# Kernel tuning notes

Measured on AMD Instinct MI355X. Metric: run time of the kernel, lower is better.

## Reference

```python
import jax, jax.numpy as jnp
import numpy as np

TOPK = 20
BN_EPS = 1e-5
NEG_SLOPE = 0.2  # DGL GAT default leaky_relu slope


def setup_inputs() -> dict:
    B, N, Ft, D = 128, 512, 64, 64
    key = jax.random.key(0)
    ks = jax.random.split(key, 6)
    return {
        "data": jax.random.normal(ks[0], (B, N, Ft), jnp.float32),
        "emb": jax.random.normal(ks[1], (N, D), jnp.float32) * 0.5,
        "fc_w": jax.random.normal(ks[2], (D, Ft), jnp.float32) * (1.0 / np.sqrt(Ft)),
        "fc_b": jnp.zeros((D,), jnp.float32),
        "attn_w": jax.random.normal(ks[3], (4 * D,), jnp.float32) * (1.0 / np.sqrt(4 * D)),
        "attn_b": jnp.zeros((), jnp.float32),
        "bn_gamma": jnp.ones((D,), jnp.float32),
        "bn_beta": jnp.zeros((D,), jnp.float32),
        "out_w": jax.random.normal(ks[4], (D,), jnp.float32) * (1.0 / np.sqrt(D)),
        "out_b": jnp.zeros((), jnp.float32),
    }


def reference(data, emb, fc_w, fc_b, attn_w, attn_b, bn_gamma, bn_beta, out_w, out_b):
    B, N, Ft = data.shape
    D = emb.shape[-1]

    # --- dynamic graph build from detached embeddings (cosine-sim topk) ---
    w = jax.lax.stop_gradient(emb)
    nrm = jnp.linalg.norm(w, axis=-1)
    cos = (w @ w.T) / (nrm[:, None] * nrm[None, :])      # [N, N]
    _, topk_idx = jax.lax.top_k(cos, TOPK)               # [N, TOPK]
    src = topk_idx.reshape(-1)                           # gated_j (message sources)
    dst = jnp.tile(jnp.arange(N), TOPK)                  # gated_i = arange(N).repeat(1,topk).flatten()

    # --- GAT layer: z = W x + b ; edge score from concat([z, emb]) at both ends ---
    z = jnp.einsum("bnf,df->bnd", data, fc_w) + fc_b     # [B, N, D]
    key_feat = jnp.concatenate([z, jnp.broadcast_to(emb, (B, N, D))], axis=-1)  # [B, N, 2D]
    a_src, a_dst = attn_w[: 2 * D], attn_w[2 * D :]
    s_src = jnp.einsum("bnd,d->bn", key_feat, a_src)
    s_dst = jnp.einsum("bnd,d->bn", key_feat, a_dst)
    e = jax.nn.leaky_relu(s_src[:, src] + s_dst[:, dst] + attn_b, NEG_SLOPE)    # [B, E]

    # segment softmax over incoming edges of each dst node (same edges every batch)
    m = jnp.full((B, N), -jnp.inf, e.dtype).at[:, dst].max(e)
    p = jnp.exp(e - m[:, dst])
    denom = jnp.zeros((B, N), e.dtype).at[:, dst].add(p)
    alpha = p / denom[:, dst]                            # [B, E]

    # scatter-aggregate messages
    h = jnp.zeros_like(z).at[:, dst].add(alpha[..., None] * z[:, src])          # [B, N, D]

    # --- trailing dense: mul by embedding, BatchNorm1d over channel D, relu, linear ---
    rst = h * emb[None]                                  # [B, N, D]
    mu = rst.mean(axis=(0, 1))
    var = rst.var(axis=(0, 1))
    rst = jax.nn.relu((rst - mu) / jnp.sqrt(var + BN_EPS) * bn_gamma + bn_beta)
    out = jnp.einsum("bnd,d->bn", rst, out_w) + out_b    # [B, N]
    return out
```

## Files before the change

kernel.cpp:

```cpp
#include <hip/hip_runtime.h>
#include <hip/hip_bf16.h>

#define NN 512
#define DD 64
#define TOPK 20
#define BB 128

__global__ __launch_bounds__(64) void k1_topk(const float* __restrict__ emb,
                                              const float* __restrict__ attn_w,
                                              int* __restrict__ topk,
                                              float* __restrict__ es_src,
                                              float* __restrict__ es_dst) {
    const int i = blockIdx.x;
    const int lane = threadIdx.x;
    const float4* e4 = (const float4*)emb;

    double dot[8] = {0,0,0,0,0,0,0,0};
    double dj [8] = {0,0,0,0,0,0,0,0};
    double di = 0.0;

    for (int c = 0; c < 16; ++c) {
        float4 wi4 = e4[i * 16 + c];
        double wx = wi4.x, wy = wi4.y, wz = wi4.z, ww = wi4.w;
        di += wx * wx; di += wy * wy; di += wz * wz; di += ww * ww;
        #pragma unroll
        for (int r = 0; r < 8; ++r) {
            float4 v = e4[(lane * 8 + r) * 16 + c];
            double vx = v.x, vy = v.y, vz = v.z, vw = v.w;
            dot[r] += wx * vx; dot[r] += wy * vy; dot[r] += wz * vz; dot[r] += ww * vw;
            dj [r] += vx * vx; dj [r] += vy * vy; dj [r] += vz * vz; dj [r] += vw * vw;
        }
    }
    const double nrm_i = sqrt(di);
    double v[8];
    #pragma unroll
    for (int r = 0; r < 8; ++r) v[r] = dot[r] / (nrm_i * sqrt(dj[r]));

    for (int k = 0; k < TOPK; ++k) {
        double bv = v[0]; int br = 0;
        #pragma unroll
        for (int r = 1; r < 8; ++r) if (v[r] > bv) { bv = v[r]; br = r; }
        int bi = lane * 8 + br;
        #pragma unroll
        for (int off = 32; off > 0; off >>= 1) {
            double ov = __shfl_xor(bv, off);
            int    oi = __shfl_xor(bi, off);
            if (ov > bv || (ov == bv && oi < bi)) { bv = ov; bi = oi; }
        }
        if (lane == 0) topk[i * TOPK + k] = bi;
        if ((bi >> 3) == lane) v[bi & 7] = -1e300;
    }

    float wf = emb[i * 64 + lane];
    float v1 = wf * attn_w[64 + lane];
    float v2 = wf * attn_w[192 + lane];
    #pragma unroll
    for (int off = 32; off > 0; off >>= 1) {
        v1 += __shfl_xor(v1, off);
        v2 += __shfl_xor(v2, off);
    }
    if (lane == 0) { es_src[i] = v1; es_dst[i] = v2; }
}

__global__ __launch_bounds__(256) void k2_gemm(const float* __restrict__ data,
                                               const float* __restrict__ fc_w,
                                               const float* __restrict__ fc_b,
                                               const float* __restrict__ attn_w,
                                               const float* __restrict__ es_src,
                                               const float* __restrict__ es_dst,
                                               float* __restrict__ z,
                                               float* __restrict__ s_src,
                                               float* __restrict__ s_dst) {
    __shared__ float As[64][65];
    __shared__ float Ws[64][65];
    __shared__ float redA[64][17];
    __shared__ float redB[64][17];
    const int t = threadIdx.x;
    const long r0 = (long)blockIdx.x * 64;

    for (int idx = t; idx < 4096; idx += 256) {
        As[idx >> 6][idx & 63] = data[r0 * 64 + idx];
        Ws[idx >> 6][idx & 63] = fc_w[idx];
    }
    __syncthreads();

    const int tr = t >> 4, tc = t & 15;
    float acc[4][4] = {};
    for (int k = 0; k < 64; ++k) {
        float a[4], b[4];
        #pragma unroll
        for (int i = 0; i < 4; ++i) a[i] = As[tr * 4 + i][k];
        #pragma unroll
        for (int j = 0; j < 4; ++j) b[j] = Ws[tc * 4 + j][k];
        #pragma unroll
        for (int i = 0; i < 4; ++i)
            #pragma unroll
            for (int j = 0; j < 4; ++j) acc[i][j] += a[i] * b[j];
    }
    float bias[4], aw0[4], aw2[4];
    #pragma unroll
    for (int j = 0; j < 4; ++j) {
        bias[j] = fc_b[tc * 4 + j];
        aw0[j]  = attn_w[tc * 4 + j];
        aw2[j]  = attn_w[128 + tc * 4 + j];
    }
    #pragma unroll
    for (int i = 0; i < 4; ++i) {
        float zb[4];
        #pragma unroll
        for (int j = 0; j < 4; ++j) zb[j] = acc[i][j] + bias[j];
        float4 vv; vv.x = zb[0]; vv.y = zb[1]; vv.z = zb[2]; vv.w = zb[3];
        *(float4*)&z[(r0 + tr * 4 + i) * 64 + tc * 4] = vv;
        float pA = zb[0] * aw0[0] + zb[1] * aw0[1] + zb[2] * aw0[2] + zb[3] * aw0[3];
        float pB = zb[0] * aw2[0] + zb[1] * aw2[1] + zb[2] * aw2[2] + zb[3] * aw2[3];
        redA[tr * 4 + i][tc] = pA;
        redB[tr * 4 + i][tc] = pB;
    }
    __syncthreads();
    if (t < 64) {
        float sA = 0.f, sB = 0.f;
        #pragma unroll
        for (int k = 0; k < 16; ++k) { sA += redA[t][k]; sB += redB[t][k]; }
        const int n = (int)((r0 + t) & (NN - 1));
        s_src[r0 + t] = sA + es_src[n];
        s_dst[r0 + t] = sB + es_dst[n];
    }
}

__global__ __launch_bounds__(256) void k3_attn(const float* __restrict__ z,
                                               const float* __restrict__ s_src,
                                               const float* __restrict__ s_dst,
                                               const int* __restrict__ topk,
                                               const float* __restrict__ emb,
                                               const float* __restrict__ attn_b_p,
                                               float* __restrict__ rst,
                                               double* __restrict__ bsum,
                                               double* __restrict__ bsum2) {
    __shared__ float  zs[512 * 16];
    __shared__ double alf_pool[2560];
    __shared__ unsigned short sIdx[256 * 20];
    float* alf = (float*)alf_pool;

    const int b   = blockIdx.x >> 2;
    const int dq  = blockIdx.x & 3;
    const int doff = dq * 16;
    const int t   = threadIdx.x;
    const float attn_b = *attn_b_p;
    const long b512 = (long)b * NN;

    float4* zs4 = (float4*)zs;
    for (int m = t; m < 2048; m += 256) {
        const int n = m >> 2, c4 = m & 3;
        zs4[m] = *(const float4*)(z + (b512 + n) * 64 + doff + c4 * 4);
    }
    __syncthreads();

    const int g = t >> 4, c = t & 15;
    double sum1 = 0.0, sum2 = 0.0;

    for (int chunk = 0; chunk < 2; ++chunk) {
        {
            const int n = chunk * 256 + t;
            const float sd = s_dst[b512 + n];
            float ev[TOPK];
            float m0 = -1e30f;
            #pragma unroll
            for (int tt = 0; tt < TOPK; ++tt) {
                const int s = topk[n + tt * NN];
                sIdx[t * TOPK + tt] = (unsigned short)s;
                float e = s_src[b512 + s] + sd + attn_b;
                e = (e >= 0.f) ? e : 0.2f * e;
                ev[tt] = e;
                m0 = fmaxf(m0, e);
            }
            float dsum = 0.f;
            #pragma unroll
            for (int tt = 0; tt < TOPK; ++tt) { ev[tt] = __expf(ev[tt] - m0); dsum += ev[tt]; }
            const float inv = 1.0f / dsum;
            #pragma unroll
            for (int tt = 0; tt < TOPK; ++tt) alf[t * TOPK + tt] = ev[tt] * inv;
        }
        __syncthreads();

        for (int it = 0; it < 16; ++it) {
            const int nl = g * 16 + it;
            const int n  = chunk * 256 + nl;
            float acc = 0.f;
            #pragma unroll
            for (int tt = 0; tt < TOPK; ++tt) {
                acc += alf[nl * TOPK + tt] * zs[(int)sIdx[nl * TOPK + tt] * 16 + c];
            }
            const float r = acc * emb[n * 64 + doff + c];
            rst[(b512 + n) * 64 + doff + c] = r;
            sum1 += (double)r;
            sum2 += (double)r * (double)r;
        }
        __syncthreads();
    }

    double* r1 = alf_pool;
    double* r2 = alf_pool + 256;
    r1[t] = sum1; r2[t] = sum2;
    __syncthreads();
    if (t < 16) {
        double a = 0.0, bb = 0.0;
        for (int g2 = 0; g2 < 16; ++g2) { a += r1[g2 * 16 + t]; bb += r2[g2 * 16 + t]; }
        bsum [blockIdx.x * 16 + t] = a;
        bsum2[blockIdx.x * 16 + t] = bb;
    }
}

__global__ __launch_bounds__(64) void k4_bn(const double* __restrict__ bsum,
                                            const double* __restrict__ bsum2,
                                            const float* __restrict__ gamma,
                                            const float* __restrict__ beta,
                                            float* __restrict__ scaleArr,
                                            float* __restrict__ biasArr) {
    const int d = threadIdx.x;
    const int dq = d >> 4, c = d & 15;
    double s = 0.0, s2 = 0.0;
    for (int b = 0; b < BB; ++b) {
        const int blk = b * 4 + dq;
        s  += bsum [blk * 16 + c];
        s2 += bsum2[blk * 16 + c];
    }
    const double M = (double)BB * (double)NN;
    const double mu  = s / M;
    const double var = s2 / M - mu * mu;
    const float scale = (float)((double)gamma[d] / sqrt(var + 1e-5));
    scaleArr[d] = scale;
    biasArr[d]  = beta[d] - (float)mu * scale;
}

__global__ __launch_bounds__(256) void k5_out(const float* __restrict__ rst,
                                              const float* __restrict__ scaleArr,
                                              const float* __restrict__ biasArr,
                                              const float* __restrict__ out_w,
                                              const float* __restrict__ out_b_p,
                                              float* __restrict__ out) {
    const int wid = threadIdx.x >> 6, lane = threadIdx.x & 63;
    const long row = (long)blockIdx.x * 4 + wid;
    const float r = rst[row * 64 + lane];
    float v = fmaxf(r * scaleArr[lane] + biasArr[lane], 0.f) * out_w[lane];
    #pragma unroll
    for (int off = 32; off > 0; off >>= 1) v += __shfl_down(v, off);
    if (lane == 0) out[row] = v + *out_b_p;
}

extern "C" void kernel_launch(void* const* d_in, const int* in_sizes, int n_in,
                              void* d_out, int out_size, void* d_ws, size_t ws_size,
                              hipStream_t stream) {
    const float* data   = (const float*)d_in[0];
    const float* emb    = (const float*)d_in[1];
    const float* fc_w   = (const float*)d_in[2];
    const float* fc_b   = (const float*)d_in[3];
    const float* attn_w = (const float*)d_in[4];
    const float* attn_b = (const float*)d_in[5];
    const float* gamma  = (const float*)d_in[6];
    const float* beta   = (const float*)d_in[7];
    const float* out_w  = (const float*)d_in[8];
    const float* out_b  = (const float*)d_in[9];
    float* out = (float*)d_out;

    char* ws = (char*)d_ws;
    const long ROWS = (long)BB * NN;
    float*  z      = (float*) (ws + 0);
    float*  rst    = (float*) (ws + 16777216);
    float*  s_src  = (float*) (ws + 33554432);
    float*  s_dst  = (float*) (ws + 33816576);
    int*    topk   = (int*)   (ws + 34078720);
    float*  es_src = (float*) (ws + 34119680);
    float*  es_dst = (float*) (ws + 34121728);
    double* bsum   = (double*)(ws + 34123776);
    double* bsum2  = (double*)(ws + 34189312);
    float*  scaleA = (float*) (ws + 34254848);
    float*  biasA  = (float*) (ws + 34255104);

    k1_topk<<<NN, 64, 0, stream>>>(emb, attn_w, topk, es_src, es_dst);
    k2_gemm<<<(int)(ROWS / 64), 256, 0, stream>>>(data, fc_w, fc_b, attn_w, es_src, es_dst,
                                                  z, s_src, s_dst);
    k3_attn<<<BB * 4, 256, 0, stream>>>(z, s_src, s_dst, topk, emb, attn_b, rst, bsum, bsum2);
    k4_bn<<<1, 64, 0, stream>>>(bsum, bsum2, gamma, beta, scaleA, biasA);
    k5_out<<<(int)(ROWS / 4), 256, 0, stream>>>(rst, scaleA, biasA, out_w, out_b, out);
}
```

Before: 165.8 us.

## Fuse topk and GEMM kernels, vectorize attention aggregation and tail kernels

Merges the cosine top-k kernel and the projection GEMM into one launch, with extra blocks handling top-k four rows per block. Because the GEMM no longer depends on the top-k output, the embedding score terms move into the attention kernel. The GEMM now uses float4 LDS reads from a transposed weight tile. The attention aggregation switches to float4 per thread with reworked BN partial reductions, the BN reduce kernel is parallelized over 512 threads, and the output kernel handles four rows per wave. These changes aim to cut launch count, serialization and memory-instruction overhead, at the cost of more complex indexing and larger shared-memory reduction buffers.

```diff
diff --git a/kernel.cpp b/kernel.cpp
--- a/kernel.cpp
+++ b/kernel.cpp
@@ -6,130 +6,141 @@
 #define TOPK 20
 #define BB 128
 
-__global__ __launch_bounds__(64) void k1_topk(const float* __restrict__ emb,
-                                              const float* __restrict__ attn_w,
-                                              int* __restrict__ topk,
-                                              float* __restrict__ es_src,
-                                              float* __restrict__ es_dst) {
-    const int i = blockIdx.x;
-    const int lane = threadIdx.x;
-    const float4* e4 = (const float4*)emb;
-
-    double dot[8] = {0,0,0,0,0,0,0,0};
-    double dj [8] = {0,0,0,0,0,0,0,0};
-    double di = 0.0;
-
-    for (int c = 0; c < 16; ++c) {
-        float4 wi4 = e4[i * 16 + c];
-        double wx = wi4.x, wy = wi4.y, wz = wi4.z, ww = wi4.w;
-        di += wx * wx; di += wy * wy; di += wz * wz; di += ww * ww;
-        #pragma unroll
-        for (int r = 0; r < 8; ++r) {
-            float4 v = e4[(lane * 8 + r) * 16 + c];
-            double vx = v.x, vy = v.y, vz = v.z, vw = v.w;
-            dot[r] += wx * vx; dot[r] += wy * vy; dot[r] += wz * vz; dot[r] += ww * vw;
-            dj [r] += vx * vx; dj [r] += vy * vy; dj [r] += vz * vz; dj [r] += vw * vw;
-        }
-    }
-    const double nrm_i = sqrt(di);
-    double v[8];
-    #pragma unroll
-    for (int r = 0; r < 8; ++r) v[r] = dot[r] / (nrm_i * sqrt(dj[r]));
-
-    for (int k = 0; k < TOPK; ++k) {
-        double bv = v[0]; int br = 0;
-        #pragma unroll
-        for (int r = 1; r < 8; ++r) if (v[r] > bv) { bv = v[r]; br = r; }
-        int bi = lane * 8 + br;
-        #pragma unroll
-        for (int off = 32; off > 0; off >>= 1) {
-            double ov = __shfl_xor(bv, off);
-            int    oi = __shfl_xor(bi, off);
-            if (ov > bv || (ov == bv && oi < bi)) { bv = ov; bi = oi; }
-        }
-        if (lane == 0) topk[i * TOPK + k] = bi;
-        if ((bi >> 3) == lane) v[bi & 7] = -1e300;
-    }
-
-    float wf = emb[i * 64 + lane];
-    float v1 = wf * attn_w[64 + lane];
-    float v2 = wf * attn_w[192 + lane];
-    #pragma unroll
-    for (int off = 32; off > 0; off >>= 1) {
-        v1 += __shfl_xor(v1, off);
-        v2 += __shfl_xor(v2, off);
-    }
-    if (lane == 0) { es_src[i] = v1; es_dst[i] = v2; }
-}
-
-__global__ __launch_bounds__(256) void k2_gemm(const float* __restrict__ data,
-                                               const float* __restrict__ fc_w,
-                                               const float* __restrict__ fc_b,
-                                               const float* __restrict__ attn_w,
-                                               const float* __restrict__ es_src,
-                                               const float* __restrict__ es_dst,
-                                               float* __restrict__ z,
-                                               float* __restrict__ s_src,
-                                               float* __restrict__ s_dst) {
-    __shared__ float As[64][65];
-    __shared__ float Ws[64][65];
+__global__ __launch_bounds__(256) void k12_fused(const float* __restrict__ data,
+                                                 const float* __restrict__ fc_w,
+                                                 const float* __restrict__ fc_b,
+                                                 const float* __restrict__ emb,
+                                                 const float* __restrict__ attn_w,
+                                                 float* __restrict__ z,
+                                                 float* __restrict__ zsrc,
+                                                 float* __restrict__ zdst,
+                                                 int* __restrict__ topk,
+                                                 float* __restrict__ es_src,
+                                                 float* __restrict__ es_dst) {
+    __shared__ float As [64][68];
+    __shared__ float WsT[64][68];
     __shared__ float redA[64][17];
     __shared__ float redB[64][17];
     const int t = threadIdx.x;
-    const long r0 = (long)blockIdx.x * 64;
-
-    for (int idx = t; idx < 4096; idx += 256) {
-        As[idx >> 6][idx & 63] = data[r0 * 64 + idx];
-        Ws[idx >> 6][idx & 63] = fc_w[idx];
-    }
-    __syncthreads();
-
-    const int tr = t >> 4, tc = t & 15;
-    float acc[4][4] = {};
-    for (int k = 0; k < 64; ++k) {
-        float a[4], b[4];
-        #pragma unroll
-        for (int i = 0; i < 4; ++i) a[i] = As[tr * 4 + i][k];
-        #pragma unroll
-        for (int j = 0; j < 4; ++j) b[j] = Ws[tc * 4 + j][k];
-        #pragma unroll
-        for (int i = 0; i < 4; ++i)
-            #pragma unroll
-            for (int j = 0; j < 4; ++j) acc[i][j] += a[i] * b[j];
-    }
-    float bias[4], aw0[4], aw2[4];
-    #pragma unroll
-    for (int j = 0; j < 4; ++j) {
-        bias[j] = fc_b[tc * 4 + j];
-        aw0[j]  = attn_w[tc * 4 + j];
-        aw2[j]  = attn_w[128 + tc * 4 + j];
-    }
-    #pragma unroll
-    for (int i = 0; i < 4; ++i) {
-        float zb[4];
-        #pragma unroll
-        for (int j = 0; j < 4; ++j) zb[j] = acc[i][j] + bias[j];
-        float4 vv; vv.x = zb[0]; vv.y = zb[1]; vv.z = zb[2]; vv.w = zb[3];
-        *(float4*)&z[(r0 + tr * 4 + i) * 64 + tc * 4] = vv;
-        float pA = zb[0] * aw0[0] + zb[1] * aw0[1] + zb[2] * aw0[2] + zb[3] * aw0[3];
-        float pB = zb[0] * aw2[0] + zb[1] * aw2[1] + zb[2] * aw2[2] + zb[3] * aw2[3];
-        redA[tr * 4 + i][tc] = pA;
-        redB[tr * 4 + i][tc] = pB;
-    }
-    __syncthreads();
-    if (t < 64) {
-        float sA = 0.f, sB = 0.f;
-        #pragma unroll
-        for (int k = 0; k < 16; ++k) { sA += redA[t][k]; sB += redB[t][k]; }
-        const int n = (int)((r0 + t) & (NN - 1));
-        s_src[r0 + t] = sA + es_src[n];
-        s_dst[r0 + t] = sB + es_dst[n];
+
+    if (blockIdx.x < 1024) {
+        const long r0 = (long)blockIdx.x * 64;
+        const float4* data4 = (const float4*)data;
+        const float4* fcw4  = (const float4*)fc_w;
+
+        for (int m = t; m < 1024; m += 256) {
+            const int r = m >> 4, c4 = m & 15;
+            *(float4*)&As[r][c4 * 4] = data4[(r0 + r) * 16 + c4];
+        }
+        for (int m = t; m < 1024; m += 256) {
+            const int d = m >> 4, f4 = m & 15;
+            float4 v = fcw4[d * 16 + f4];
+            WsT[f4 * 4 + 0][d] = v.x;
+            WsT[f4 * 4 + 1][d] = v.y;
+            WsT[f4 * 4 + 2][d] = v.z;
+            WsT[f4 * 4 + 3][d] = v.w;
+        }
+        __syncthreads();
+
+        const int tr = t >> 4, tc = t & 15;
+        float acc[4][4] = {};
+        for (int k0 = 0; k0 < 64; k0 += 4) {
+            float4 a4[4], b4[4];
+            #pragma unroll
+            for (int i = 0; i < 4; ++i) a4[i] = *(float4*)&As[tr * 4 + i][k0];
+            #pragma unroll
+            for (int kk = 0; kk < 4; ++kk) b4[kk] = *(float4*)&WsT[k0 + kk][tc * 4];
+            #pragma unroll
+            for (int i = 0; i < 4; ++i) {
+                acc[i][0] += a4[i].x * b4[0].x + a4[i].y * b4[1].x + a4[i].z * b4[2].x + a4[i].w * b4[3].x;
+                acc[i][1] += a4[i].x * b4[0].y + a4[i].y * b4[1].y + a4[i].z * b4[2].y + a4[i].w * b4[3].y;
+                acc[i][2] += a4[i].x * b4[0].z + a4[i].y * b4[1].z + a4[i].z * b4[2].z + a4[i].w * b4[3].z;
+                acc[i][3] += a4[i].x * b4[0].w + a4[i].y * b4[1].w + a4[i].z * b4[2].w + a4[i].w * b4[3].w;
+            }
+        }
+        float bias[4], aw0[4], aw2[4];
+        #pragma unroll
+        for (int j = 0; j < 4; ++j) {
+            bias[j] = fc_b[tc * 4 + j];
+            aw0[j]  = attn_w[tc * 4 + j];
+            aw2[j]  = attn_w[128 + tc * 4 + j];
+        }
+        #pragma unroll
+        for (int i = 0; i < 4; ++i) {
+            float zb[4];
+            #pragma unroll
+            for (int j = 0; j < 4; ++j) zb[j] = acc[i][j] + bias[j];
+            float4 vv; vv.x = zb[0]; vv.y = zb[1]; vv.z = zb[2]; vv.w = zb[3];
+            *(float4*)&z[(r0 + tr * 4 + i) * 64 + tc * 4] = vv;
+            redA[tr * 4 + i][tc] = zb[0] * aw0[0] + zb[1] * aw0[1] + zb[2] * aw0[2] + zb[3] * aw0[3];
+            redB[tr * 4 + i][tc] = zb[0] * aw2[0] + zb[1] * aw2[1] + zb[2] * aw2[2] + zb[3] * aw2[3];
+        }
+        __syncthreads();
+        if (t < 64) {
+            float sA = 0.f, sB = 0.f;
+            #pragma unroll
+            for (int k = 0; k < 16; ++k) { sA += redA[t][k]; sB += redB[t][k]; }
+            zsrc[r0 + t] = sA;
+            zdst[r0 + t] = sB;
+        }
+    } else {
+        const int i = (blockIdx.x - 1024) * 4 + (t >> 6);
+        const int lane = t & 63;
+        const float4* e4 = (const float4*)emb;
+
+        double dot[8] = {0,0,0,0,0,0,0,0};
+        double dj [8] = {0,0,0,0,0,0,0,0};
+        double di = 0.0;
+
+        for (int c = 0; c < 16; ++c) {
+            float4 wi4 = e4[i * 16 + c];
+            double wx = wi4.x, wy = wi4.y, wz = wi4.z, ww = wi4.w;
+            di += wx * wx; di += wy * wy; di += wz * wz; di += ww * ww;
+            #pragma unroll
+            for (int r = 0; r < 8; ++r) {
+                float4 v = e4[(lane * 8 + r) * 16 + c];
+                double vx = v.x, vy = v.y, vz = v.z, vw = v.w;
+                dot[r] += wx * vx; dot[r] += wy * vy; dot[r] += wz * vz; dot[r] += ww * vw;
+                dj [r] += vx * vx; dj [r] += vy * vy; dj [r] += vz * vz; dj [r] += vw * vw;
+            }
+        }
+        const double nrm_i = sqrt(di);
+        double v[8];
+        #pragma unroll
+        for (int r = 0; r < 8; ++r) v[r] = dot[r] / (nrm_i * sqrt(dj[r]));
+
+        for (int k = 0; k < TOPK; ++k) {
+            double bv = v[0]; int br = 0;
+            #pragma unroll
+            for (int r = 1; r < 8; ++r) if (v[r] > bv) { bv = v[r]; br = r; }
+            int bi = lane * 8 + br;
+            #pragma unroll
+            for (int off = 32; off > 0; off >>= 1) {
+                double ov = __shfl_xor(bv, off);
+                int    oi = __shfl_xor(bi, off);
+                if (ov > bv || (ov == bv && oi < bi)) { bv = ov; bi = oi; }
+            }
+            if (lane == 0) topk[i * TOPK + k] = bi;
+            if ((bi >> 3) == lane) v[bi & 7] = -1e300;
+        }
+
+        float wf = emb[i * 64 + lane];
+        float v1 = wf * attn_w[64 + lane];
+        float v2 = wf * attn_w[192 + lane];
+        #pragma unroll
+        for (int off = 32; off > 0; off >>= 1) {
+            v1 += __shfl_xor(v1, off);
+            v2 += __shfl_xor(v2, off);
+        }
+        if (lane == 0) { es_src[i] = v1; es_dst[i] = v2; }
     }
 }
 
 __global__ __launch_bounds__(256) void k3_attn(const float* __restrict__ z,
-                                               const float* __restrict__ s_src,
-                                               const float* __restrict__ s_dst,
+                                               const float* __restrict__ zsrc,
+                                               const float* __restrict__ zdst,
+                                               const float* __restrict__ es_src,
+                                               const float* __restrict__ es_dst,
                                                const int* __restrict__ topk,
                                                const float* __restrict__ emb,
                                                const float* __restrict__ attn_b_p,
@@ -141,10 +152,10 @@
     __shared__ unsigned short sIdx[256 * 20];
     float* alf = (float*)alf_pool;
 
-    const int b   = blockIdx.x >> 2;
-    const int dq  = blockIdx.x & 3;
+    const int b    = blockIdx.x >> 2;
+    const int dq   = blockIdx.x & 3;
     const int doff = dq * 16;
-    const int t   = threadIdx.x;
+    const int t    = threadIdx.x;
     const float attn_b = *attn_b_p;
     const long b512 = (long)b * NN;
 
@@ -155,20 +166,21 @@
     }
     __syncthreads();
 
-    const int g = t >> 4, c = t & 15;
-    double sum1 = 0.0, sum2 = 0.0;
+    const int c4 = t & 3;
+    const int rq = t >> 2;
+    double s1[4] = {0,0,0,0}, s2[4] = {0,0,0,0};
 
     for (int chunk = 0; chunk < 2; ++chunk) {
         {
             const int n = chunk * 256 + t;
-            const float sd = s_dst[b512 + n];
+            const float sd = zdst[b512 + n] + es_dst[n] + attn_b;
             float ev[TOPK];
             float m0 = -1e30f;
             #pragma unroll
             for (int tt = 0; tt < TOPK; ++tt) {
                 const int s = topk[n + tt * NN];
                 sIdx[t * TOPK + tt] = (unsigned short)s;
-                float e = s_src[b512 + s] + sd + attn_b;
+                float e = zsrc[b512 + s] + es_src[s] + sd;
                 e = (e >= 0.f) ? e : 0.2f * e;
                 ev[tt] = e;
                 m0 = fmaxf(m0, e);
@@ -182,54 +194,74 @@
         }
         __syncthreads();
 
-        for (int it = 0; it < 16; ++it) {
-            const int nl = g * 16 + it;
+        #pragma unroll
+        for (int it = 0; it < 4; ++it) {
+            const int nl = it * 64 + rq;
             const int n  = chunk * 256 + nl;
-            float acc = 0.f;
+            float4 acc = {0.f, 0.f, 0.f, 0.f};
             #pragma unroll
             for (int tt = 0; tt < TOPK; ++tt) {
-                acc += alf[nl * TOPK + tt] * zs[(int)sIdx[nl * TOPK + tt] * 16 + c];
-            }
-            const float r = acc * emb[n * 64 + doff + c];
-            rst[(b512 + n) * 64 + doff + c] = r;
-            sum1 += (double)r;
-            sum2 += (double)r * (double)r;
+                const float a = alf[nl * TOPK + tt];
+                const float4 zv = zs4[(int)sIdx[nl * TOPK + tt] * 4 + c4];
+                acc.x += a * zv.x; acc.y += a * zv.y; acc.z += a * zv.z; acc.w += a * zv.w;
+            }
+            const float4 ev = *(const float4*)&emb[n * 64 + doff + c4 * 4];
+            float4 r;
+            r.x = acc.x * ev.x; r.y = acc.y * ev.y; r.z = acc.z * ev.z; r.w = acc.w * ev.w;
+            *(float4*)&rst[(b512 + n) * 64 + doff + c4 * 4] = r;
+            s1[0] += (double)r.x; s2[0] += (double)r.x * (double)r.x;
+            s1[1] += (double)r.y; s2[1] += (double)r.y * (double)r.y;
+            s1[2] += (double)r.z; s2[2] += (double)r.z * (double)r.z;
+            s1[3] += (double)r.w; s2[3] += (double)r.w * (double)r.w;
         }
         __syncthreads();
     }
 
     double* r1 = alf_pool;
-    double* r2 = alf_pool + 256;
-    r1[t] = sum1; r2[t] = sum2;
+    double* r2 = alf_pool + 1024;
+    #pragma unroll
+    for (int j = 0; j < 4; ++j) {
+        r1[(c4 * 4 + j) * 64 + rq] = s1[j];
+        r2[(c4 * 4 + j) * 64 + rq] = s2[j];
+    }
     __syncthreads();
     if (t < 16) {
         double a = 0.0, bb = 0.0;
-        for (int g2 = 0; g2 < 16; ++g2) { a += r1[g2 * 16 + t]; bb += r2[g2 * 16 + t]; }
+        for (int q = 0; q < 64; ++q) { a += r1[t * 64 + q]; bb += r2[t * 64 + q]; }
         bsum [blockIdx.x * 16 + t] = a;
         bsum2[blockIdx.x * 16 + t] = bb;
     }
 }
 
-__global__ __launch_bounds__(64) void k4_bn(const double* __restrict__ bsum,
-                                            const double* __restrict__ bsum2,
-                                            const float* __restrict__ gamma,
-                                            const float* __restrict__ beta,
-                                            float* __restrict__ scaleArr,
-                                            float* __restrict__ biasArr) {
-    const int d = threadIdx.x;
+__global__ __launch_bounds__(512) void k4_bn(const double* __restrict__ bsum,
+                                             const double* __restrict__ bsum2,
+                                             const float* __restrict__ gamma,
+                                             const float* __restrict__ beta,
+                                             float* __restrict__ scaleArr,
+                                             float* __restrict__ biasArr) {
+    __shared__ double r1[512], r2[512];
+    const int t = threadIdx.x;
+    const int d = t & 63, part = t >> 6;
     const int dq = d >> 4, c = d & 15;
     double s = 0.0, s2 = 0.0;
-    for (int b = 0; b < BB; ++b) {
+    for (int b = part; b < BB; b += 8) {
         const int blk = b * 4 + dq;
         s  += bsum [blk * 16 + c];
         s2 += bsum2[blk * 16 + c];
     }
-    const double M = (double)BB * (double)NN;
-    const double mu  = s / M;
-    const double var = s2 / M - mu * mu;
-    const float scale = (float)((double)gamma[d] / sqrt(var + 1e-5));
-    scaleArr[d] = scale;
-    biasArr[d]  = beta[d] - (float)mu * scale;
+    r1[part * 64 + d] = s; r2[part * 64 + d] = s2;
+    __syncthreads();
+    if (t < 64) {
+        double S = 0.0, S2 = 0.0;
+        #pragma unroll
+        for (int p = 0; p < 8; ++p) { S += r1[p * 64 + t]; S2 += r2[p * 64 + t]; }
+        const double M = (double)BB * (double)NN;
+        const double mu  = S / M;
+        const double var = S2 / M - mu * mu;
+        const float scale = (float)((double)gamma[t] / sqrt(var + 1e-5));
+        scaleArr[t] = scale;
+        biasArr[t]  = beta[t] - (float)mu * scale;
+    }
 }
 
 __global__ __launch_bounds__(256) void k5_out(const float* __restrict__ rst,
@@ -239,12 +271,20 @@
                                               const float* __restrict__ out_b_p,
                                               float* __restrict__ out) {
     const int wid = threadIdx.x >> 6, lane = threadIdx.x & 63;
-    const long row = (long)blockIdx.x * 4 + wid;
-    const float r = rst[row * 64 + lane];
-    float v = fmaxf(r * scaleArr[lane] + biasArr[lane], 0.f) * out_w[lane];
+    const float sc = scaleArr[lane], bi = biasArr[lane], ow = out_w[lane];
+    const float ob = *out_b_p;
+    const long rowbase = (long)blockIdx.x * 16 + wid * 4;
+    float v[4];
     #pragma unroll
-    for (int off = 32; off > 0; off >>= 1) v += __shfl_down(v, off);
-    if (lane == 0) out[row] = v + *out_b_p;
+    for (int rr = 0; rr < 4; ++rr)
+        v[rr] = fmaxf(rst[(rowbase + rr) * 64 + lane] * sc + bi, 0.f) * ow;
+    #pragma unroll
+    for (int off = 32; off > 0; off >>= 1)
+        #pragma unroll
+        for (int rr = 0; rr < 4; ++rr) v[rr] += __shfl_down(v[rr], off);
+    if (lane == 0)
+        #pragma unroll
+        for (int rr = 0; rr < 4; ++rr) out[rowbase + rr] = v[rr] + ob;
 }
 
 extern "C" void kernel_launch(void* const* d_in, const int* in_sizes, int n_in,
@@ -263,11 +303,10 @@
     float* out = (float*)d_out;
 
     char* ws = (char*)d_ws;
-    const long ROWS = (long)BB * NN;
     float*  z      = (float*) (ws + 0);
     float*  rst    = (float*) (ws + 16777216);
-    float*  s_src  = (float*) (ws + 33554432);
-    float*  s_dst  = (float*) (ws + 33816576);
+    float*  zsrc   = (float*) (ws + 33554432);
+    float*  zdst   = (float*) (ws + 33816576);
     int*    topk   = (int*)   (ws + 34078720);
     float*  es_src = (float*) (ws + 34119680);
     float*  es_dst = (float*) (ws + 34121728);
@@ -276,10 +315,10 @@
     float*  scaleA = (float*) (ws + 34254848);
     float*  biasA  = (float*) (ws + 34255104);
 
-    k1_topk<<<NN, 64, 0, stream>>>(emb, attn_w, topk, es_src, es_dst);
-    k2_gemm<<<(int)(ROWS / 64), 256, 0, stream>>>(data, fc_w, fc_b, attn_w, es_src, es_dst,
-                                                  z, s_src, s_dst);
-    k3_attn<<<BB * 4, 256, 0, stream>>>(z, s_src, s_dst, topk, emb, attn_b, rst, bsum, bsum2);
-    k4_bn<<<1, 64, 0, stream>>>(bsum, bsum2, gamma, beta, scaleA, biasA);
-    k5_out<<<(int)(ROWS / 4), 256, 0, stream>>>(rst, scaleA, biasA, out_w, out_b, out);
-}
+    k12_fused<<<1152, 256, 0, stream>>>(data, fc_w, fc_b, emb, attn_w,
+                                        z, zsrc, zdst, topk, es_src, es_dst);
+    k3_attn<<<BB * 4, 256, 0, stream>>>(z, zsrc, zdst, es_src, es_dst, topk, emb,
+                                        attn_b, rst, bsum, bsum2);
+    k4_bn<<<1, 512, 0, stream>>>(bsum, bsum2, gamma, beta, scaleA, biasA);
+    k5_out<<<4096, 256, 0, stream>>>(rst, scaleA, biasA, out_w, out_b, out);
+}
```

Result: slower. 170.4 us (+2.8%).
